# Optimization experiments

Measured on AMD Instinct MI355X. Metric: run time of the kernel, lower is better.

Reference implementation:

```python
import jax, jax.numpy as jnp
import numpy as np

NUM_CLASSES = 512  # static number of distinct labels (all present in targets)
EPS = 1e-8         # torch.nn.CosineSimilarity default eps


def setup_inputs() -> dict:
    N, D, C = 65536, 256, NUM_CLASSES
    key = jax.random.key(0)
    k1, k2 = jax.random.split(key)
    inputs = jax.random.normal(k1, (N, D), dtype=jnp.float32)
    # every label 0..C-1 appears -> sorted-unique remap in the torch code is identity
    targets = jax.random.permutation(k2, jnp.arange(N, dtype=jnp.int32) % C)
    return {"inputs": inputs, "targets": targets}


def reference(inputs, targets):
    C = NUM_CLASSES
    # per-label segment mean (prototypes), replacing the python unique/mask loop
    sums = jax.ops.segment_sum(inputs, targets, num_segments=C)          # [C, D]
    counts = jax.ops.segment_sum(jnp.ones((inputs.shape[0],), inputs.dtype),
                                 targets, num_segments=C)                # [C]
    protos = sums / counts[:, None]                                       # [C, D]

    # pairwise cosine similarity: x.p / max(|x||p|, eps)
    dots = inputs @ protos.T                                              # [N, C]
    n_in = jnp.linalg.norm(inputs, axis=-1)                               # [N]
    n_pr = jnp.linalg.norm(protos, axis=-1)                               # [C]
    sim = dots / jnp.maximum(n_in[:, None] * n_pr[None, :], EPS)          # [N, C]

    # cross entropy, mean reduction (labels already equal mapped targets)
    logp = jax.nn.log_softmax(sim, axis=-1)                               # [N, C]
    nll = -jnp.take_along_axis(logp, targets[:, None].astype(jnp.int32), axis=-1)[:, 0]
    return jnp.mean(nll)
```

## Files before the change

kernel.cpp:

```cpp
#include <hip/hip_runtime.h>
#include <math.h>

#define NROWS 65536
#define DIM   256
#define NCLS  512
#define CPW   128
#define BM    64
#define NBLK  1024

#define WS_CNT_I   0
#define WS_IDX_I   512
#define WS_QPACK_F 66048

typedef float f32x4  __attribute__((ext_vector_type(4)));
typedef short bf16x8 __attribute__((ext_vector_type(8)));
typedef unsigned short u16;

__device__ inline u16 f2bf(float f) {
  unsigned u = __float_as_uint(f);
  u += 0x7FFFu + ((u >> 16) & 1u);
  return (u16)(u >> 16);
}
__device__ inline unsigned pack2(float a, float b) {
  return (unsigned)f2bf(a) | ((unsigned)f2bf(b) << 16);
}

__global__ __launch_bounds__(512) void k_zero(int* __restrict__ cnt,
                                              float* __restrict__ out) {
  cnt[threadIdx.x] = 0;
  if (threadIdx.x == 0) out[0] = 0.f;
}

__global__ __launch_bounds__(256) void k_scatter(
    const int* __restrict__ tgt, int* __restrict__ cnt, int* __restrict__ idx) {
  const int row = blockIdx.x * 256 + threadIdx.x;
  const int c = tgt[row];
  const int p = atomicAdd(&cnt[c], 1);
  if (p < CPW) idx[c * CPW + p] = row;
}

__global__ __launch_bounds__(512) void k_csum(
    const float* __restrict__ x, const int* __restrict__ idx,
    u16* __restrict__ qpack) {
  __shared__ int   sidx[CPW];
  __shared__ float wpart[8][DIM];
  __shared__ float wsum[4];
  __shared__ float ninv_s;
  const int c    = blockIdx.x;
  const int tid  = threadIdx.x;
  const int w    = tid >> 6;
  const int lane = tid & 63;
  if (tid < CPW) sidx[tid] = idx[c * CPW + tid];
  __syncthreads();

  float4 a4[4];
  #pragma unroll
  for (int j = 0; j < 4; ++j) a4[j] = make_float4(0.f, 0.f, 0.f, 0.f);
  #pragma unroll
  for (int i = 0; i < 4; ++i) {
    #pragma unroll
    for (int j = 0; j < 4; ++j) {
      const int row = sidx[w * 16 + i * 4 + j];
      const float4 v = *reinterpret_cast<const float4*>(
          x + (size_t)row * DIM + lane * 4);
      a4[j].x += v.x; a4[j].y += v.y; a4[j].z += v.z; a4[j].w += v.w;
    }
  }
  float4 vs;
  vs.x = (a4[0].x + a4[1].x) + (a4[2].x + a4[3].x);
  vs.y = (a4[0].y + a4[1].y) + (a4[2].y + a4[3].y);
  vs.z = (a4[0].z + a4[1].z) + (a4[2].z + a4[3].z);
  vs.w = (a4[0].w + a4[1].w) + (a4[2].w + a4[3].w);
  *reinterpret_cast<float4*>(&wpart[w][lane * 4]) = vs;
  __syncthreads();

  float s = 0.f;
  if (tid < DIM) {
    #pragma unroll
    for (int ww = 0; ww < 8; ++ww) s += wpart[ww][tid];
  }
  float sq = s * s;
  sq += __shfl_xor(sq, 1, 64);
  sq += __shfl_xor(sq, 2, 64);
  sq += __shfl_xor(sq, 4, 64);
  sq += __shfl_xor(sq, 8, 64);
  sq += __shfl_xor(sq, 16, 64);
  sq += __shfl_xor(sq, 32, 64);
  if (tid < DIM && (tid & 63) == 0) wsum[tid >> 6] = sq;
  __syncthreads();
  if (tid == 0) ninv_s = rsqrtf(fmaxf(wsum[0] + wsum[1] + wsum[2] + wsum[3], 1e-30f));
  __syncthreads();
  if (tid < DIM)
    qpack[((tid >> 3) * NCLS + c) * 8 + (tid & 7)] = f2bf(s * ninv_s);
}

__global__ __launch_bounds__(512) void k_main(
    const float* __restrict__ x, const int* __restrict__ tgt,
    const u16* __restrict__ qpack, float* __restrict__ out) {
  __shared__ u16   Alds[32 * 64 * 8] __attribute__((aligned(16)));
  __shared__ float psum[8][64];
  __shared__ float simt[64];
  __shared__ int   ltgt[64];

  const int tid  = threadIdx.x;
  const int t    = blockIdx.x;
  const int w    = tid >> 6;
  const int lane = tid & 63;

  {
    const int row  = tid >> 3;
    const int part = tid & 7;
    const float4* xr = reinterpret_cast<const float4*>(
        x + (size_t)(t * BM + row) * DIM + part * 32);
    float4 v[8];
    #pragma unroll
    for (int j = 0; j < 8; ++j) v[j] = xr[j];
    float ss = 0.f;
    #pragma unroll
    for (int j = 0; j < 8; ++j)
      ss += v[j].x * v[j].x + v[j].y * v[j].y + v[j].z * v[j].z + v[j].w * v[j].w;
    ss += __shfl_xor(ss, 1, 64);
    ss += __shfl_xor(ss, 2, 64);
    ss += __shfl_xor(ss, 4, 64);
    const float rn = rsqrtf(fmaxf(ss, 1e-30f));
    #pragma unroll
    for (int jj = 0; jj < 4; ++jj) {
      uint4 wv;
      wv.x = pack2(v[2*jj].x * rn,   v[2*jj].y * rn);
      wv.y = pack2(v[2*jj].z * rn,   v[2*jj].w * rn);
      wv.z = pack2(v[2*jj+1].x * rn, v[2*jj+1].y * rn);
      wv.w = pack2(v[2*jj+1].z * rn, v[2*jj+1].w * rn);
      const int kg = part * 4 + jj;
      const int rs = row ^ part;
      *reinterpret_cast<uint4*>(&Alds[(kg * 64 + rs) * 8]) = wv;
    }
  }
  if (tid < BM) ltgt[tid] = tgt[t * BM + tid];
  __syncthreads();

  const int lg = lane >> 4, l15 = lane & 15;
  f32x4 acc[4][4];
  #pragma unroll
  for (int m = 0; m < 4; ++m)
    #pragma unroll
    for (int n = 0; n < 4; ++n) acc[m][n] = (f32x4)0.f;

  const bf16x8* bp = reinterpret_cast<const bf16x8*>(qpack);
  const int bbase = w * 64 + l15;

  bf16x8 b0[4], b1[4];
  #pragma unroll
  for (int n = 0; n < 4; ++n) b0[n] = bp[lg * NCLS + bbase + n * 16];

  #pragma unroll 1
  for (int kk = 0; kk < 8; kk += 2) {
    #pragma unroll
    for (int n = 0; n < 4; ++n)
      b1[n] = bp[((kk + 1) * 4 + lg) * NCLS + bbase + n * 16];
    {
      bf16x8 a[4];
      #pragma unroll
      for (int m = 0; m < 4; ++m)
        a[m] = *reinterpret_cast<const bf16x8*>(
            &Alds[((kk * 4 + lg) * 64 + ((m * 16 + l15) ^ kk)) * 8]);
      #pragma unroll
      for (int m = 0; m < 4; ++m)
        #pragma unroll
        for (int n = 0; n < 4; ++n)
          acc[m][n] = __builtin_amdgcn_mfma_f32_16x16x32_bf16(a[m], b0[n], acc[m][n], 0, 0, 0);
    }
    const int k2 = (kk + 2) & 7;
    #pragma unroll
    for (int n = 0; n < 4; ++n)
      b0[n] = bp[(k2 * 4 + lg) * NCLS + bbase + n * 16];
    {
      bf16x8 a[4];
      #pragma unroll
      for (int m = 0; m < 4; ++m)
        a[m] = *reinterpret_cast<const bf16x8*>(
            &Alds[(((kk + 1) * 4 + lg) * 64 + ((m * 16 + l15) ^ (kk + 1))) * 8]);
      #pragma unroll
      for (int m = 0; m < 4; ++m)
        #pragma unroll
        for (int n = 0; n < 4; ++n)
          acc[m][n] = __builtin_amdgcn_mfma_f32_16x16x32_bf16(a[m], b1[n], acc[m][n], 0, 0, 0);
    }
  }

  #pragma unroll
  for (int m = 0; m < 4; ++m) {
    #pragma unroll
    for (int reg = 0; reg < 4; ++reg) {
      const int r = m * 16 + lg * 4 + reg;
      float s = __expf(acc[m][0][reg]) + __expf(acc[m][1][reg]) +
                __expf(acc[m][2][reg]) + __expf(acc[m][3][reg]);
      s += __shfl_xor(s, 1, 64);
      s += __shfl_xor(s, 2, 64);
      s += __shfl_xor(s, 4, 64);
      s += __shfl_xor(s, 8, 64);
      if (l15 == 0) psum[w][r] = s;
      const int tg = ltgt[r];
      if (w == (tg >> 6) && l15 == (tg & 15)) {
        const int nt = (tg >> 4) & 3;
        float pv = acc[m][0][reg];
        pv = (nt == 1) ? acc[m][1][reg] : pv;
        pv = (nt == 2) ? acc[m][2][reg] : pv;
        pv = (nt == 3) ? acc[m][3][reg] : pv;
        simt[r] = pv;
      }
    }
  }
  __syncthreads();
  if (tid < 64) {
    float sum = 0.f;
    #pragma unroll
    for (int ww = 0; ww < 8; ++ww) sum += psum[ww][tid];
    float lr = __logf(sum) - simt[tid];
    lr += __shfl_xor(lr, 1, 64);
    lr += __shfl_xor(lr, 2, 64);
    lr += __shfl_xor(lr, 4, 64);
    lr += __shfl_xor(lr, 8, 64);
    lr += __shfl_xor(lr, 16, 64);
    lr += __shfl_xor(lr, 32, 64);
    if (tid == 0) atomicAdd(out, lr * (1.0f / (float)NROWS));
  }
}

extern "C" void kernel_launch(void* const* d_in, const int* in_sizes, int n_in,
                              void* d_out, int out_size, void* d_ws, size_t ws_size,
                              hipStream_t stream) {
  const float* x   = (const float*)d_in[0];
  const int*   tgt = (const int*)d_in[1];
  float* ws    = (float*)d_ws;
  int*   cnt   = (int*)ws + WS_CNT_I;
  int*   idx   = (int*)ws + WS_IDX_I;
  u16*   qpack = (u16*)(ws + WS_QPACK_F);
  float* out   = (float*)d_out;

  k_zero<<<1, 512, 0, stream>>>(cnt, out);
  k_scatter<<<NROWS / 256, 256, 0, stream>>>(tgt, cnt, idx);
  k_csum<<<NCLS, 512, 0, stream>>>(x, idx, qpack);
  k_main<<<NBLK, 512, 0, stream>>>(x, tgt, qpack, out);
}
```

Measured before the change: 79.12 us.

## Process four 64-row subtiles per block with prototypes held in registers

Each main-kernel block now loops over four 64-row subtiles. The full per-wave slice of the bf16 prototype matrix is loaded into registers once and reused across all four subtiles, rather than being streamed from global memory for every 64-row tile. The per-block loss is accumulated and written with a single atomic per block, and the grid shrinks to a quarter of its previous size. In exchange, the 128-register B cache plus the accumulators may spill under the 512x2 launch bound. The smaller grid of roughly one block per CU also removes the latency hiding that more resident blocks provided, because each block's loads and MFMA work now run serially.

```diff
diff --git a/kernel.cpp b/kernel.cpp
--- a/kernel.cpp
+++ b/kernel.cpp
@@ -5,8 +5,9 @@
 #define DIM   256
 #define NCLS  512
 #define CPW   128
-#define BM    64
-#define NBLK  1024
+#define BMAIN 256
+#define NSUB  4
+#define NBLK  (NROWS / BMAIN)
 
 #define WS_CNT_I   0
 #define WS_IDX_I   512
@@ -94,7 +95,7 @@
     qpack[((tid >> 3) * NCLS + c) * 8 + (tid & 7)] = f2bf(s * ninv_s);
 }
 
-__global__ __launch_bounds__(512) void k_main(
+__global__ __launch_bounds__(512, 2) void k_main(
     const float* __restrict__ x, const int* __restrict__ tgt,
     const u16* __restrict__ qpack, float* __restrict__ out) {
   __shared__ u16   Alds[32 * 64 * 8] __attribute__((aligned(16)));
@@ -103,61 +104,64 @@
   __shared__ int   ltgt[64];
 
   const int tid  = threadIdx.x;
-  const int t    = blockIdx.x;
   const int w    = tid >> 6;
   const int lane = tid & 63;
-
-  {
-    const int row  = tid >> 3;
-    const int part = tid & 7;
-    const float4* xr = reinterpret_cast<const float4*>(
-        x + (size_t)(t * BM + row) * DIM + part * 32);
-    float4 v[8];
-    #pragma unroll
-    for (int j = 0; j < 8; ++j) v[j] = xr[j];
-    float ss = 0.f;
-    #pragma unroll
-    for (int j = 0; j < 8; ++j)
-      ss += v[j].x * v[j].x + v[j].y * v[j].y + v[j].z * v[j].z + v[j].w * v[j].w;
-    ss += __shfl_xor(ss, 1, 64);
-    ss += __shfl_xor(ss, 2, 64);
-    ss += __shfl_xor(ss, 4, 64);
-    const float rn = rsqrtf(fmaxf(ss, 1e-30f));
-    #pragma unroll
-    for (int jj = 0; jj < 4; ++jj) {
-      uint4 wv;
-      wv.x = pack2(v[2*jj].x * rn,   v[2*jj].y * rn);
-      wv.y = pack2(v[2*jj].z * rn,   v[2*jj].w * rn);
-      wv.z = pack2(v[2*jj+1].x * rn, v[2*jj+1].y * rn);
-      wv.w = pack2(v[2*jj+1].z * rn, v[2*jj+1].w * rn);
-      const int kg = part * 4 + jj;
-      const int rs = row ^ part;
-      *reinterpret_cast<uint4*>(&Alds[(kg * 64 + rs) * 8]) = wv;
-    }
-  }
-  if (tid < BM) ltgt[tid] = tgt[t * BM + tid];
-  __syncthreads();
-
-  const int lg = lane >> 4, l15 = lane & 15;
-  f32x4 acc[4][4];
-  #pragma unroll
-  for (int m = 0; m < 4; ++m)
-    #pragma unroll
-    for (int n = 0; n < 4; ++n) acc[m][n] = (f32x4)0.f;
+  const int lg   = lane >> 4, l15 = lane & 15;
+  const int row  = tid >> 3;
+  const int part = tid & 7;
 
   const bf16x8* bp = reinterpret_cast<const bf16x8*>(qpack);
   const int bbase = w * 64 + l15;
-
-  bf16x8 b0[4], b1[4];
+  bf16x8 B[8][4];
   #pragma unroll
-  for (int n = 0; n < 4; ++n) b0[n] = bp[lg * NCLS + bbase + n * 16];
+  for (int kk = 0; kk < 8; ++kk)
+    #pragma unroll
+    for (int n = 0; n < 4; ++n)
+      B[kk][n] = bp[(kk * 4 + lg) * NCLS + bbase + n * 16];
+
+  float block_loss = 0.f;
 
   #pragma unroll 1
-  for (int kk = 0; kk < 8; kk += 2) {
-    #pragma unroll
-    for (int n = 0; n < 4; ++n)
-      b1[n] = bp[((kk + 1) * 4 + lg) * NCLS + bbase + n * 16];
+  for (int s = 0; s < NSUB; ++s) {
+    const int r0 = blockIdx.x * BMAIN + s * 64;
+
     {
+      const float4* xr = reinterpret_cast<const float4*>(
+          x + (size_t)(r0 + row) * DIM + part * 32);
+      float4 v[8];
+      #pragma unroll
+      for (int j = 0; j < 8; ++j) v[j] = xr[j];
+      float ss = 0.f;
+      #pragma unroll
+      for (int j = 0; j < 8; ++j)
+        ss += v[j].x * v[j].x + v[j].y * v[j].y + v[j].z * v[j].z + v[j].w * v[j].w;
+      ss += __shfl_xor(ss, 1, 64);
+      ss += __shfl_xor(ss, 2, 64);
+      ss += __shfl_xor(ss, 4, 64);
+      const float rn = rsqrtf(fmaxf(ss, 1e-30f));
+      #pragma unroll
+      for (int jj = 0; jj < 4; ++jj) {
+        uint4 wv;
+        wv.x = pack2(v[2*jj].x * rn,   v[2*jj].y * rn);
+        wv.y = pack2(v[2*jj].z * rn,   v[2*jj].w * rn);
+        wv.z = pack2(v[2*jj+1].x * rn, v[2*jj+1].y * rn);
+        wv.w = pack2(v[2*jj+1].z * rn, v[2*jj+1].w * rn);
+        const int kg = part * 4 + jj;
+        const int rs = row ^ part;
+        *reinterpret_cast<uint4*>(&Alds[(kg * 64 + rs) * 8]) = wv;
+      }
+    }
+    if (tid < 64) ltgt[tid] = tgt[r0 + tid];
+    __syncthreads();
+
+    f32x4 acc[4][4];
+    #pragma unroll
+    for (int m = 0; m < 4; ++m)
+      #pragma unroll
+      for (int n = 0; n < 4; ++n) acc[m][n] = (f32x4)0.f;
+
+    #pragma unroll
+    for (int kk = 0; kk < 8; ++kk) {
       bf16x8 a[4];
       #pragma unroll
       for (int m = 0; m < 4; ++m)
@@ -167,63 +171,48 @@
       for (int m = 0; m < 4; ++m)
         #pragma unroll
         for (int n = 0; n < 4; ++n)
-          acc[m][n] = __builtin_amdgcn_mfma_f32_16x16x32_bf16(a[m], b0[n], acc[m][n], 0, 0, 0);
-    }
-    const int k2 = (kk + 2) & 7;
-    #pragma unroll
-    for (int n = 0; n < 4; ++n)
-      b0[n] = bp[(k2 * 4 + lg) * NCLS + bbase + n * 16];
-    {
-      bf16x8 a[4];
-      #pragma unroll
-      for (int m = 0; m < 4; ++m)
-        a[m] = *reinterpret_cast<const bf16x8*>(
-            &Alds[(((kk + 1) * 4 + lg) * 64 + ((m * 16 + l15) ^ (kk + 1))) * 8]);
-      #pragma unroll
-      for (int m = 0; m < 4; ++m)
-        #pragma unroll
-        for (int n = 0; n < 4; ++n)
-          acc[m][n] = __builtin_amdgcn_mfma_f32_16x16x32_bf16(a[m], b1[n], acc[m][n], 0, 0, 0);
+          acc[m][n] = __builtin_amdgcn_mfma_f32_16x16x32_bf16(a[m], B[kk][n], acc[m][n], 0, 0, 0);
+    }
+
+    #pragma unroll
+    for (int m = 0; m < 4; ++m) {
+      #pragma unroll
+      for (int reg = 0; reg < 4; ++reg) {
+        const int r = m * 16 + lg * 4 + reg;
+        float sx = __expf(acc[m][0][reg]) + __expf(acc[m][1][reg]) +
+                   __expf(acc[m][2][reg]) + __expf(acc[m][3][reg]);
+        sx += __shfl_xor(sx, 1, 64);
+        sx += __shfl_xor(sx, 2, 64);
+        sx += __shfl_xor(sx, 4, 64);
+        sx += __shfl_xor(sx, 8, 64);
+        if (l15 == 0) psum[w][r] = sx;
+        const int tg = ltgt[r];
+        if (w == (tg >> 6) && l15 == (tg & 15)) {
+          const int nt = (tg >> 4) & 3;
+          float pv = acc[m][0][reg];
+          pv = (nt == 1) ? acc[m][1][reg] : pv;
+          pv = (nt == 2) ? acc[m][2][reg] : pv;
+          pv = (nt == 3) ? acc[m][3][reg] : pv;
+          simt[r] = pv;
+        }
+      }
+    }
+    __syncthreads();
+    if (tid < 64) {
+      float sum = 0.f;
+      #pragma unroll
+      for (int ww = 0; ww < 8; ++ww) sum += psum[ww][tid];
+      float lr = __logf(sum) - simt[tid];
+      lr += __shfl_xor(lr, 1, 64);
+      lr += __shfl_xor(lr, 2, 64);
+      lr += __shfl_xor(lr, 4, 64);
+      lr += __shfl_xor(lr, 8, 64);
+      lr += __shfl_xor(lr, 16, 64);
+      lr += __shfl_xor(lr, 32, 64);
+      block_loss += lr;
     }
   }
-
-  #pragma unroll
-  for (int m = 0; m < 4; ++m) {
-    #pragma unroll
-    for (int reg = 0; reg < 4; ++reg) {
-      const int r = m * 16 + lg * 4 + reg;
-      float s = __expf(acc[m][0][reg]) + __expf(acc[m][1][reg]) +
-                __expf(acc[m][2][reg]) + __expf(acc[m][3][reg]);
-      s += __shfl_xor(s, 1, 64);
-      s += __shfl_xor(s, 2, 64);
-      s += __shfl_xor(s, 4, 64);
-      s += __shfl_xor(s, 8, 64);
-      if (l15 == 0) psum[w][r] = s;
-      const int tg = ltgt[r];
-      if (w == (tg >> 6) && l15 == (tg & 15)) {
-        const int nt = (tg >> 4) & 3;
-        float pv = acc[m][0][reg];
-        pv = (nt == 1) ? acc[m][1][reg] : pv;
-        pv = (nt == 2) ? acc[m][2][reg] : pv;
-        pv = (nt == 3) ? acc[m][3][reg] : pv;
-        simt[r] = pv;
-      }
-    }
-  }
-  __syncthreads();
-  if (tid < 64) {
-    float sum = 0.f;
-    #pragma unroll
-    for (int ww = 0; ww < 8; ++ww) sum += psum[ww][tid];
-    float lr = __logf(sum) - simt[tid];
-    lr += __shfl_xor(lr, 1, 64);
-    lr += __shfl_xor(lr, 2, 64);
-    lr += __shfl_xor(lr, 4, 64);
-    lr += __shfl_xor(lr, 8, 64);
-    lr += __shfl_xor(lr, 16, 64);
-    lr += __shfl_xor(lr, 32, 64);
-    if (tid == 0) atomicAdd(out, lr * (1.0f / (float)NROWS));
-  }
+  if (tid == 0) atomicAdd(out, block_loss * (1.0f / (float)NROWS));
 }
 
 extern "C" void kernel_launch(void* const* d_in, const int* in_sizes, int n_in,
```

After: 84.64 us. 7.0% more time.
